# Kernel optimization log

Hardware: AMD Instinct MI355X
Metric: run time of the kernel (lower is better)

## Reference

```python
import jax, jax.numpy as jnp
import numpy as np

D_MODEL = 1024
N_HEAD = 16
D_K = 64
D_V = 64
LN_EPS = 1e-5


def setup_inputs() -> dict:
    key = jax.random.key(0)
    ks = jax.random.split(key, 12)
    B, S = 4, 2048
    s = 1.0 / np.sqrt(D_MODEL)
    inp = {
        "q": jax.random.normal(ks[0], (B, S, D_MODEL), jnp.float32),
        "k": jax.random.normal(ks[1], (B, S, D_MODEL), jnp.float32),
        "v": jax.random.normal(ks[2], (B, S, D_MODEL), jnp.float32),
        "mask": jnp.ones((B, S, S), jnp.int32),
        "w_q": jax.random.normal(ks[3], (D_MODEL, N_HEAD * D_K), jnp.float32) * s,
        "b_q": jnp.zeros((N_HEAD * D_K,), jnp.float32),
        "w_k": jax.random.normal(ks[4], (D_MODEL, N_HEAD * D_K), jnp.float32) * s,
        "b_k": jnp.zeros((N_HEAD * D_K,), jnp.float32),
        "w_v": jax.random.normal(ks[5], (D_MODEL, N_HEAD * D_V), jnp.float32) * s,
        "b_v": jnp.zeros((N_HEAD * D_V,), jnp.float32),
        "w_fc": jax.random.normal(ks[6], (N_HEAD * D_V, D_MODEL), jnp.float32) * s,
        "b_fc": jnp.zeros((D_MODEL,), jnp.float32),
        "ln_g": jnp.ones((D_MODEL,), jnp.float32),
        "ln_b": jnp.zeros((D_MODEL,), jnp.float32),
    }
    return inp


def reference(q, k, v, mask, w_q, b_q, w_k, b_k, w_v, b_v, w_fc, b_fc, ln_g, ln_b):
    B, Sq, _ = q.shape
    Sk = k.shape[1]
    residual = q
    # QKV projections -> [B, H, S, d]
    qh = (q @ w_q + b_q).reshape(B, Sq, N_HEAD, D_K).transpose(0, 2, 1, 3)
    kh = (k @ w_k + b_k).reshape(B, Sk, N_HEAD, D_K).transpose(0, 2, 1, 3)
    vh = (v @ w_v + b_v).reshape(B, Sk, N_HEAD, D_V).transpose(0, 2, 1, 3)
    temp = jnp.sqrt(jnp.asarray(D_K, qh.dtype))
    scores = jnp.einsum("bhqd,bhkd->bhqk", qh / temp, kh)
    scores = jnp.where(mask[:, None, :, :] == 0, jnp.asarray(-1e9, scores.dtype), scores)
    attn = jax.nn.softmax(scores, axis=-1)  # dropout is identity in eval
    out = jnp.einsum("bhqk,bhkd->bhqd", attn, vh)
    out = out.transpose(0, 2, 1, 3).reshape(B, Sq, N_HEAD * D_V)
    out = out @ w_fc + b_fc  # output proj (dropout identity)
    x = out + residual
    mu = jnp.mean(x, axis=-1, keepdims=True)
    var = jnp.mean(jnp.square(x - mu), axis=-1, keepdims=True)
    y = (x - mu) * jax.lax.rsqrt(var + LN_EPS) * ln_g + ln_b
    return (y, attn)
```

## Files before the change

kernel.cpp:

```cpp
#include <hip/hip_runtime.h>
#include <cstdint>
#include <cstddef>

#define DM 1024
#define HN 16
#define DH 64
#define BB 4
#define SS 2048
#define MM (BB * SS)

typedef __bf16 bf16;
typedef bf16 bf16x8 __attribute__((ext_vector_type(8)));
typedef bf16 bf16x4 __attribute__((ext_vector_type(4)));
typedef float f32x4 __attribute__((ext_vector_type(4)));

__device__ __forceinline__ f32x4 mfma16(bf16x8 a, bf16x8 b, f32x4 c) {
  return __builtin_amdgcn_mfma_f32_16x16x32_bf16(a, b, c, 0, 0, 0);
}

typedef __attribute__((address_space(3))) void lds_void_t;
typedef __attribute__((address_space(1))) void glob_void_t;

__device__ __forceinline__ void gload16(const void* g, void* l) {
  __builtin_amdgcn_global_load_lds((const glob_void_t*)g, (lds_void_t*)l, 16, 0, 0);
}

__global__ __launch_bounds__(256) void cvt_f2b(const float* __restrict__ in,
                                               bf16* __restrict__ out) {
  int i = (blockIdx.x * 256 + threadIdx.x) * 8;
  f32x4 a = *(const f32x4*)(in + i);
  f32x4 b = *(const f32x4*)(in + i + 4);
  bf16x8 o;
  o[0] = (bf16)a[0]; o[1] = (bf16)a[1]; o[2] = (bf16)a[2]; o[3] = (bf16)a[3];
  o[4] = (bf16)b[0]; o[5] = (bf16)b[1]; o[6] = (bf16)b[2]; o[7] = (bf16)b[3];
  *(bf16x8*)(out + i) = o;
}

__global__ __launch_bounds__(256) void wtrans(const float* __restrict__ W,
                                              bf16* __restrict__ WT) {
  __shared__ float t[32][33];
  int n0 = blockIdx.x * 32, k0 = blockIdx.y * 32;
  int tid = threadIdx.x;
  int r = tid >> 3, c = (tid & 7) * 4;
  f32x4 v = *(const f32x4*)&W[(size_t)(k0 + r) * DM + n0 + c];
  t[r][c] = v[0]; t[r][c + 1] = v[1]; t[r][c + 2] = v[2]; t[r][c + 3] = v[3];
  __syncthreads();
  bf16x4 o;
#pragma unroll
  for (int i = 0; i < 4; ++i) o[i] = (bf16)t[c + i][r];
  *(bf16x4*)&WT[(size_t)(n0 + r) * DM + k0 + c] = o;
}

__global__ __launch_bounds__(256) void vtrans(const bf16* __restrict__ vh,
                                              bf16* __restrict__ vhT) {
  __shared__ bf16 t[256][72];
  int bh = blockIdx.y, s0 = blockIdx.x * 256;
  const bf16* src = vh + (size_t)bh * SS * DH;
  bf16* dst = vhT + (size_t)bh * SS * DH;
  int tid = threadIdx.x;
#pragma unroll
  for (int j = 0; j < 8; ++j)
    *(bf16x8*)&t[tid][j * 8] = *(const bf16x8*)&src[(size_t)(s0 + tid) * DH + j * 8];
  __syncthreads();
  int d = tid >> 2, cc = (tid & 3) * 64;
#pragma unroll
  for (int j = 0; j < 8; ++j) {
    bf16x8 o;
#pragma unroll
    for (int i = 0; i < 8; ++i) o[i] = t[cc + j * 8 + i][d];
    *(bf16x8*)&dst[(size_t)d * SS + s0 + cc + j * 8] = o;
  }
}

template <int MODE>
__global__ __launch_bounds__(256) void gemm128(const bf16* __restrict__ A,
                                               const bf16* __restrict__ Bt,
                                               const float* __restrict__ bias,
                                               const float* __restrict__ resid,
                                               void* __restrict__ out) {
  constexpr int K = DM;
  __shared__ bf16 Ab[128 * 32];
  __shared__ bf16 Bb[128 * 32];
  int tid = threadIdx.x, wave = tid >> 6, lane = tid & 63;
  int bm = blockIdx.x * 128, bn = blockIdx.y * 128;
  int wr = (wave >> 1) * 64, wc = (wave & 1) * 64;
  int fr = lane & 15, kg8 = (lane >> 4) * 8;
  f32x4 acc[4][4] = {};
  int arow = tid >> 2, acol = (tid & 3) * 8;
  const bf16* Ag0 = A + (size_t)(bm + arow) * K + acol;
  const bf16* Ag1 = Ag0 + (size_t)64 * K;
  const bf16* Bg0 = Bt + (size_t)(bn + arow) * K + acol;
  const bf16* Bg1 = Bg0 + (size_t)64 * K;
  char* la = (char*)Ab + wave * 1024;
  char* lb = (char*)Bb + wave * 1024;
  for (int k0 = 0; k0 < K; k0 += 32) {
    __syncthreads();
    gload16(Ag0 + k0, la);
    gload16(Ag1 + k0, la + 4096);
    gload16(Bg0 + k0, lb);
    gload16(Bg1 + k0, lb + 4096);
    asm volatile("s_waitcnt vmcnt(0)" ::: "memory");
    __syncthreads();
    bf16x8 af[4], bfr[4];
#pragma unroll
    for (int m = 0; m < 4; ++m)
      af[m] = *(const bf16x8*)&Ab[(wr + m * 16 + fr) * 32 + kg8];
#pragma unroll
    for (int n = 0; n < 4; ++n)
      bfr[n] = *(const bf16x8*)&Bb[(wc + n * 16 + fr) * 32 + kg8];
#pragma unroll
    for (int m = 0; m < 4; ++m)
#pragma unroll
      for (int n = 0; n < 4; ++n) acc[m][n] = mfma16(af[m], bfr[n], acc[m][n]);
  }
#pragma unroll
  for (int m = 0; m < 4; ++m)
#pragma unroll
    for (int n = 0; n < 4; ++n) {
      int c = bn + wc + n * 16 + fr;
      float bv = bias[c];
#pragma unroll
      for (int j = 0; j < 4; ++j) {
        int r = bm + wr + m * 16 + (lane >> 4) * 4 + j;
        float v = acc[m][n][j] + bv;
        if (MODE == 0) {
          size_t idx = (size_t)((r >> 11) * HN + (c >> 6)) * (SS * DH) +
                       (size_t)(r & (SS - 1)) * DH + (c & (DH - 1));
          ((bf16*)out)[idx] = (bf16)v;
        } else {
          size_t idx = (size_t)r * DM + c;
          ((float*)out)[idx] = v + resid[idx];
        }
      }
    }
}

__global__ __launch_bounds__(512) void attn_kernel(const bf16* __restrict__ qh,
                                                   const bf16* __restrict__ kh,
                                                   const bf16* __restrict__ vhT,
                                                   const int* __restrict__ mask,
                                                   float* __restrict__ attn_out,
                                                   bf16* __restrict__ ctx) {
  extern __shared__ char smem[];
  float* pbuf = (float*)(smem + 16 * 4096);
  float* invp = (float*)(smem + 16 * 4096 + 4096);
  int tid = threadIdx.x, wave = tid >> 6, lane = tid & 63;
  int qt = blockIdx.x, bh = blockIdx.y;
  int b = bh >> 4, h = bh & 15;
  int q0 = qt * 16;
  const bf16* qbase = qh + ((size_t)bh * SS + q0) * DH;
  const bf16* kbase = kh + (size_t)bh * SS * DH;
  const bf16* vbase = vhT + (size_t)bh * SS * DH;
  int fr = lane & 15, kg = lane >> 4;

  bf16x8 qf0 = *(const bf16x8*)&qbase[(size_t)fr * DH + kg * 8];
  bf16x8 qf1 = *(const bf16x8*)&qbase[(size_t)fr * DH + 32 + kg * 8];

  int sw = wave * 256;
  const int* mrow = mask + ((size_t)b * SS + q0) * SS;
  for (int s0 = sw; s0 < sw + 256; s0 += 16) {
    f32x4 acc = {0.f, 0.f, 0.f, 0.f};
    bf16x8 kf0 = *(const bf16x8*)&kbase[(size_t)(s0 + fr) * DH + kg * 8];
    bf16x8 kf1 = *(const bf16x8*)&kbase[(size_t)(s0 + fr) * DH + 32 + kg * 8];
    acc = mfma16(qf0, kf0, acc);
    acc = mfma16(qf1, kf1, acc);
    int col = s0 + fr;
    int slot = col >> 3, within = col & 7;
#pragma unroll
    for (int j = 0; j < 4; ++j) {
      int row = kg * 4 + j;
      float v = acc[j] * 0.125f;
      if (mrow[(size_t)row * SS + col] == 0) v = -1e9f;
      *(bf16*)(smem + row * 4096 + ((slot ^ row) << 4) + within * 2) = (bf16)v;
    }
  }
  __syncthreads();

  {
    int row = wave * 2 + (lane >> 5);
    int la = lane & 31;
    char* rbase = smem + row * 4096;
    int rm = row;
    float mx = -1e30f;
#pragma unroll 2
    for (int it = 0; it < 8; ++it) {
      int slot = la + it * 32;
      bf16x8 e = *(const bf16x8*)(rbase + ((slot ^ rm) << 4));
#pragma unroll
      for (int i = 0; i < 8; ++i) mx = fmaxf(mx, (float)e[i]);
    }
#pragma unroll
    for (int off = 1; off < 32; off <<= 1) mx = fmaxf(mx, __shfl_xor(mx, off));
    float sum = 0.f;
#pragma unroll 2
    for (int it = 0; it < 8; ++it) {
      int slot = la + it * 32;
      char* p = rbase + ((slot ^ rm) << 4);
      bf16x8 e = *(const bf16x8*)p;
      bf16x8 w8;
#pragma unroll
      for (int i = 0; i < 8; ++i) {
        float f = __expf((float)e[i] - mx);
        sum += f;
        w8[i] = (bf16)f;
      }
      *(bf16x8*)p = w8;
    }
#pragma unroll
    for (int off = 1; off < 32; off <<= 1) sum += __shfl_xor(sum, off);
    float inv = 1.f / sum;
    if (la == 0) invp[row] = inv;
    float* arow_ = attn_out + ((size_t)bh * SS + q0 + row) * SS;
#pragma unroll 2
    for (int it = 0; it < 8; ++it) {
      int slot = la + it * 32;
      bf16x8 e = *(const bf16x8*)(rbase + ((slot ^ rm) << 4));
      f32x4 u0, u1;
#pragma unroll
      for (int i = 0; i < 4; ++i) {
        u0[i] = (float)e[i] * inv;
        u1[i] = (float)e[i + 4] * inv;
      }
      __builtin_nontemporal_store(u0, (f32x4*)&arow_[slot * 8]);
      __builtin_nontemporal_store(u1, (f32x4*)&arow_[slot * 8 + 4]);
    }
  }
  __syncthreads();

  {
    int dq = wave & 3, khalf = wave >> 2;
    f32x4 cacc = {0.f, 0.f, 0.f, 0.f};
    const bf16* vrow = vbase + (size_t)(dq * 16 + fr) * SS;
    char* prow = smem + fr * 4096;
    int prm = fr;
    for (int k0 = khalf * 1024; k0 < khalf * 1024 + 1024; k0 += 32) {
      int slotA = (k0 >> 3) + kg;
      bf16x8 pa = *(const bf16x8*)(prow + ((slotA ^ prm) << 4));
      bf16x8 vf = *(const bf16x8*)&vrow[k0 + kg * 8];
      cacc = mfma16(pa, vf, cacc);
    }
    if (khalf == 1) {
#pragma unroll
      for (int j = 0; j < 4; ++j)
        pbuf[dq * 256 + (kg * 4 + j) * 16 + fr] = cacc[j];
    }
    __syncthreads();
    if (khalf == 0) {
#pragma unroll
      for (int j = 0; j < 4; ++j) {
        int row = kg * 4 + j;
        float v = (cacc[j] + pbuf[dq * 256 + row * 16 + fr]) * invp[row];
        ctx[((size_t)b * SS + q0 + row) * DM + h * DH + dq * 16 + fr] = (bf16)v;
      }
    }
  }
}

__global__ __launch_bounds__(256) void ln_k(float* __restrict__ x,
                                            const float* __restrict__ g,
                                            const float* __restrict__ bln) {
  int r = blockIdx.x, tid = threadIdx.x;
  f32x4 v = *(const f32x4*)&x[(size_t)r * DM + tid * 4];
  float s = v[0] + v[1] + v[2] + v[3];
  float s2 = v[0] * v[0] + v[1] * v[1] + v[2] * v[2] + v[3] * v[3];
#pragma unroll
  for (int off = 32; off; off >>= 1) {
    s += __shfl_down(s, off);
    s2 += __shfl_down(s2, off);
  }
  __shared__ float rs_[4], rs2_[4];
  int wave = tid >> 6, lane = tid & 63;
  if (lane == 0) {
    rs_[wave] = s;
    rs2_[wave] = s2;
  }
  __syncthreads();
  s = rs_[0] + rs_[1] + rs_[2] + rs_[3];
  s2 = rs2_[0] + rs2_[1] + rs2_[2] + rs2_[3];
  float mu = s * (1.f / DM);
  float var = s2 * (1.f / DM) - mu * mu;
  float rstd = rsqrtf(var + 1e-5f);
  f32x4 gg = *(const f32x4*)&g[tid * 4];
  f32x4 bb = *(const f32x4*)&bln[tid * 4];
  f32x4 o;
#pragma unroll
  for (int i = 0; i < 4; ++i) o[i] = (v[i] - mu) * rstd * gg[i] + bb[i];
  *(f32x4*)&x[(size_t)r * DM + tid * 4] = o;
}

extern "C" void kernel_launch(void* const* d_in, const int* in_sizes, int n_in,
                              void* d_out, int out_size, void* d_ws,
                              size_t ws_size, hipStream_t stream) {
  const float* q = (const float*)d_in[0];
  const float* k = (const float*)d_in[1];
  const float* v = (const float*)d_in[2];
  const int* mask = (const int*)d_in[3];
  const float* w_q = (const float*)d_in[4];
  const float* b_q = (const float*)d_in[5];
  const float* w_k = (const float*)d_in[6];
  const float* b_k = (const float*)d_in[7];
  const float* w_v = (const float*)d_in[8];
  const float* b_v = (const float*)d_in[9];
  const float* w_fc = (const float*)d_in[10];
  const float* b_fc = (const float*)d_in[11];
  const float* ln_g = (const float*)d_in[12];
  const float* ln_b = (const float*)d_in[13];

  float* y = (float*)d_out;
  float* attn_out = (float*)d_out + (size_t)MM * DM;

  char* w = (char*)d_ws;
  const size_t actN = (size_t)MM * DM;
  bf16* q_bf = (bf16*)w;  w += actN * 2;
  bf16* k_bf = (bf16*)w;  w += actN * 2;
  bf16* v_bf = (bf16*)w;  w += actN * 2;
  bf16* wqT = (bf16*)w;   w += (size_t)DM * DM * 2;
  bf16* wkT = (bf16*)w;   w += (size_t)DM * DM * 2;
  bf16* wvT = (bf16*)w;   w += (size_t)DM * DM * 2;
  bf16* wfcT = (bf16*)w;  w += (size_t)DM * DM * 2;
  bf16* qhh = (bf16*)w;   w += actN * 2;
  bf16* khh = (bf16*)w;   w += actN * 2;
  bf16* vhh = (bf16*)w;   w += actN * 2;
  bf16* vhT = (bf16*)w;   w += actN * 2;
  bf16* ctx = (bf16*)w;   w += actN * 2;

  cvt_f2b<<<4096, 256, 0, stream>>>(q, q_bf);
  cvt_f2b<<<4096, 256, 0, stream>>>(k, k_bf);
  cvt_f2b<<<4096, 256, 0, stream>>>(v, v_bf);
  dim3 wg(DM / 32, DM / 32);
  wtrans<<<wg, 256, 0, stream>>>(w_q, wqT);
  wtrans<<<wg, 256, 0, stream>>>(w_k, wkT);
  wtrans<<<wg, 256, 0, stream>>>(w_v, wvT);
  wtrans<<<wg, 256, 0, stream>>>(w_fc, wfcT);
  dim3 gg(MM / 128, DM / 128);
  gemm128<0><<<gg, 256, 0, stream>>>(q_bf, wqT, b_q, nullptr, qhh);
  gemm128<0><<<gg, 256, 0, stream>>>(k_bf, wkT, b_k, nullptr, khh);
  gemm128<0><<<gg, 256, 0, stream>>>(v_bf, wvT, b_v, nullptr, vhh);
  vtrans<<<dim3(SS / 256, BB * HN), 256, 0, stream>>>(vhh, vhT);
  hipFuncSetAttribute((const void*)attn_kernel,
                      hipFuncAttributeMaxDynamicSharedMemorySize, 69696);
  attn_kernel<<<dim3(SS / 16, BB * HN), 512, 69696, stream>>>(
      qhh, khh, vhT, mask, attn_out, ctx);
  gemm128<1><<<gg, 256, 0, stream>>>(ctx, wfcT, b_fc, q, (void*)y);
  ln_k<<<MM, 256, 0, stream>>>(y, ln_g, ln_b);
}
```

Baseline: 805.2 us.

## Batch QKV projection, fuse V transpose, drop softmax max pass, prefetch attention loads

Merges the three input conversions, four weight transposes and three QKV GEMMs into single launches, with the GEMM picking its projection from the column block. The V projection epilogue writes the transposed layout directly, which removes the separate vtrans kernel, and the 1/8 scale is folded into Q. The softmax drops the max-subtraction pass and applies the mask as vectorized int loads in the exp pass. The QK and PV loops are software-pipelined with register prefetch, and the attention kernel gets an occupancy hint in its launch bounds. Skipping the max subtraction risks overflow for large scores, and a fully masked row would now divide by zero instead of giving a uniform distribution.

Result: faster. 759.0 us (-5.7%).

```diff
diff --git a/kernel.cpp b/kernel.cpp
--- a/kernel.cpp
+++ b/kernel.cpp
@@ -13,6 +13,7 @@
 typedef bf16 bf16x8 __attribute__((ext_vector_type(8)));
 typedef bf16 bf16x4 __attribute__((ext_vector_type(4)));
 typedef float f32x4 __attribute__((ext_vector_type(4)));
+typedef int i32x4 __attribute__((ext_vector_type(4)));
 
 __device__ __forceinline__ f32x4 mfma16(bf16x8 a, bf16x8 b, f32x4 c) {
   return __builtin_amdgcn_mfma_f32_16x16x32_bf16(a, b, c, 0, 0, 0);
@@ -25,8 +26,13 @@
   __builtin_amdgcn_global_load_lds((const glob_void_t*)g, (lds_void_t*)l, 16, 0, 0);
 }
 
-__global__ __launch_bounds__(256) void cvt_f2b(const float* __restrict__ in,
-                                               bf16* __restrict__ out) {
+__global__ __launch_bounds__(256) void cvt3(const float* __restrict__ q,
+                                            const float* __restrict__ k,
+                                            const float* __restrict__ v,
+                                            bf16* __restrict__ dst) {
+  int which = blockIdx.y;
+  const float* in = which == 0 ? q : which == 1 ? k : v;
+  bf16* out = dst + (size_t)which * MM * DM;
   int i = (blockIdx.x * 256 + threadIdx.x) * 8;
   f32x4 a = *(const f32x4*)(in + i);
   f32x4 b = *(const f32x4*)(in + i + 4);
@@ -36,8 +42,14 @@
   *(bf16x8*)(out + i) = o;
 }
 
-__global__ __launch_bounds__(256) void wtrans(const float* __restrict__ W,
-                                              bf16* __restrict__ WT) {
+__global__ __launch_bounds__(256) void wtrans4(const float* __restrict__ w_q,
+                                               const float* __restrict__ w_k,
+                                               const float* __restrict__ w_v,
+                                               const float* __restrict__ w_fc,
+                                               bf16* __restrict__ WT) {
+  int p = blockIdx.z;
+  const float* W = p == 0 ? w_q : p == 1 ? w_k : p == 2 ? w_v : w_fc;
+  bf16* out = WT + (size_t)p * DM * DM;
   __shared__ float t[32][33];
   int n0 = blockIdx.x * 32, k0 = blockIdx.y * 32;
   int tid = threadIdx.x;
@@ -48,36 +60,89 @@
   bf16x4 o;
 #pragma unroll
   for (int i = 0; i < 4; ++i) o[i] = (bf16)t[c + i][r];
-  *(bf16x4*)&WT[(size_t)(n0 + r) * DM + k0 + c] = o;
-}
-
-__global__ __launch_bounds__(256) void vtrans(const bf16* __restrict__ vh,
-                                              bf16* __restrict__ vhT) {
-  __shared__ bf16 t[256][72];
-  int bh = blockIdx.y, s0 = blockIdx.x * 256;
-  const bf16* src = vh + (size_t)bh * SS * DH;
-  bf16* dst = vhT + (size_t)bh * SS * DH;
-  int tid = threadIdx.x;
-#pragma unroll
-  for (int j = 0; j < 8; ++j)
-    *(bf16x8*)&t[tid][j * 8] = *(const bf16x8*)&src[(size_t)(s0 + tid) * DH + j * 8];
-  __syncthreads();
-  int d = tid >> 2, cc = (tid & 3) * 64;
-#pragma unroll
-  for (int j = 0; j < 8; ++j) {
-    bf16x8 o;
-#pragma unroll
-    for (int i = 0; i < 8; ++i) o[i] = t[cc + j * 8 + i][d];
-    *(bf16x8*)&dst[(size_t)d * SS + s0 + cc + j * 8] = o;
-  }
-}
-
-template <int MODE>
-__global__ __launch_bounds__(256) void gemm128(const bf16* __restrict__ A,
-                                               const bf16* __restrict__ Bt,
-                                               const float* __restrict__ bias,
-                                               const float* __restrict__ resid,
-                                               void* __restrict__ out) {
+  *(bf16x4*)&out[(size_t)(n0 + r) * DM + k0 + c] = o;
+}
+
+__global__ __launch_bounds__(256) void gemm_qkv(const bf16* __restrict__ Abase,
+                                                const bf16* __restrict__ Bt,
+                                                const float* __restrict__ b_q,
+                                                const float* __restrict__ b_k,
+                                                const float* __restrict__ b_v,
+                                                bf16* __restrict__ qhh,
+                                                bf16* __restrict__ khh,
+                                                bf16* __restrict__ vhT) {
+  constexpr int K = DM;
+  __shared__ bf16 Ab[128 * 32];
+  __shared__ bf16 Bb[128 * 32];
+  int tid = threadIdx.x, wave = tid >> 6, lane = tid & 63;
+  int bm = blockIdx.x * 128, bn = blockIdx.y * 128;
+  int proj = bn >> 10;
+  const bf16* A = Abase + (size_t)proj * MM * DM;
+  const float* bias = proj == 0 ? b_q : proj == 1 ? b_k : b_v;
+  int wr = (wave >> 1) * 64, wc = (wave & 1) * 64;
+  int fr = lane & 15, kg8 = (lane >> 4) * 8;
+  f32x4 acc[4][4] = {};
+  int arow = tid >> 2, acol = (tid & 3) * 8;
+  const bf16* Ag0 = A + (size_t)(bm + arow) * K + acol;
+  const bf16* Ag1 = Ag0 + (size_t)64 * K;
+  const bf16* Bg0 = Bt + (size_t)(bn + arow) * K + acol;
+  const bf16* Bg1 = Bg0 + (size_t)64 * K;
+  char* la = (char*)Ab + wave * 1024;
+  char* lb = (char*)Bb + wave * 1024;
+  for (int k0 = 0; k0 < K; k0 += 32) {
+    __syncthreads();
+    gload16(Ag0 + k0, la);
+    gload16(Ag1 + k0, la + 4096);
+    gload16(Bg0 + k0, lb);
+    gload16(Bg1 + k0, lb + 4096);
+    asm volatile("s_waitcnt vmcnt(0)" ::: "memory");
+    __syncthreads();
+    bf16x8 af[4], bfr[4];
+#pragma unroll
+    for (int m = 0; m < 4; ++m)
+      af[m] = *(const bf16x8*)&Ab[(wr + m * 16 + fr) * 32 + kg8];
+#pragma unroll
+    for (int n = 0; n < 4; ++n)
+      bfr[n] = *(const bf16x8*)&Bb[(wc + n * 16 + fr) * 32 + kg8];
+#pragma unroll
+    for (int m = 0; m < 4; ++m)
+#pragma unroll
+      for (int n = 0; n < 4; ++n) acc[m][n] = mfma16(af[m], bfr[n], acc[m][n]);
+  }
+  int b = bm >> 11;
+#pragma unroll
+  for (int m = 0; m < 4; ++m)
+#pragma unroll
+    for (int n = 0; n < 4; ++n) {
+      int c = bn + wc + n * 16 + fr;
+      int lc = c & 1023;
+      float bv = bias[lc];
+      int h = lc >> 6, d = lc & 63;
+      int r0 = bm + wr + m * 16 + (lane >> 4) * 4;
+      int s0 = r0 & (SS - 1);
+      if (proj == 2) {
+        bf16x4 o;
+#pragma unroll
+        for (int j = 0; j < 4; ++j) o[j] = (bf16)(acc[m][n][j] + bv);
+        *(bf16x4*)&vhT[((size_t)(b * HN + h) * DH + d) * SS + s0] = o;
+      } else {
+        bf16* dst = proj == 0 ? qhh : khh;
+        float sc = proj == 0 ? 0.125f : 1.f;
+#pragma unroll
+        for (int j = 0; j < 4; ++j) {
+          float v = (acc[m][n][j] + bv) * sc;
+          dst[(size_t)(b * HN + h) * (SS * DH) + (size_t)(s0 + j) * DH + d] =
+              (bf16)v;
+        }
+      }
+    }
+}
+
+__global__ __launch_bounds__(256) void gemm_out(const bf16* __restrict__ A,
+                                                const bf16* __restrict__ Bt,
+                                                const float* __restrict__ bias,
+                                                const float* __restrict__ resid,
+                                                float* __restrict__ out) {
   constexpr int K = DM;
   __shared__ bf16 Ab[128 * 32];
   __shared__ bf16 Bb[128 * 32];
@@ -122,25 +187,16 @@
 #pragma unroll
       for (int j = 0; j < 4; ++j) {
         int r = bm + wr + m * 16 + (lane >> 4) * 4 + j;
-        float v = acc[m][n][j] + bv;
-        if (MODE == 0) {
-          size_t idx = (size_t)((r >> 11) * HN + (c >> 6)) * (SS * DH) +
-                       (size_t)(r & (SS - 1)) * DH + (c & (DH - 1));
-          ((bf16*)out)[idx] = (bf16)v;
-        } else {
-          size_t idx = (size_t)r * DM + c;
-          ((float*)out)[idx] = v + resid[idx];
-        }
-      }
-    }
-}
-
-__global__ __launch_bounds__(512) void attn_kernel(const bf16* __restrict__ qh,
-                                                   const bf16* __restrict__ kh,
-                                                   const bf16* __restrict__ vhT,
-                                                   const int* __restrict__ mask,
-                                                   float* __restrict__ attn_out,
-                                                   bf16* __restrict__ ctx) {
+        size_t idx = (size_t)r * DM + c;
+        out[idx] = acc[m][n][j] + bv + resid[idx];
+      }
+    }
+}
+
+__global__ __launch_bounds__(512, 4) void attn_kernel(
+    const bf16* __restrict__ qh, const bf16* __restrict__ kh,
+    const bf16* __restrict__ vhT, const int* __restrict__ mask,
+    float* __restrict__ attn_out, bf16* __restrict__ ctx) {
   extern __shared__ char smem[];
   float* pbuf = (float*)(smem + 16 * 4096);
   float* invp = (float*)(smem + 16 * 4096 + 4096);
@@ -156,22 +212,31 @@
   bf16x8 qf0 = *(const bf16x8*)&qbase[(size_t)fr * DH + kg * 8];
   bf16x8 qf1 = *(const bf16x8*)&qbase[(size_t)fr * DH + 32 + kg * 8];
 
-  int sw = wave * 256;
-  const int* mrow = mask + ((size_t)b * SS + q0) * SS;
-  for (int s0 = sw; s0 < sw + 256; s0 += 16) {
-    f32x4 acc = {0.f, 0.f, 0.f, 0.f};
-    bf16x8 kf0 = *(const bf16x8*)&kbase[(size_t)(s0 + fr) * DH + kg * 8];
-    bf16x8 kf1 = *(const bf16x8*)&kbase[(size_t)(s0 + fr) * DH + 32 + kg * 8];
-    acc = mfma16(qf0, kf0, acc);
-    acc = mfma16(qf1, kf1, acc);
-    int col = s0 + fr;
-    int slot = col >> 3, within = col & 7;
-#pragma unroll
-    for (int j = 0; j < 4; ++j) {
-      int row = kg * 4 + j;
-      float v = acc[j] * 0.125f;
-      if (mrow[(size_t)row * SS + col] == 0) v = -1e9f;
-      *(bf16*)(smem + row * 4096 + ((slot ^ row) << 4) + within * 2) = (bf16)v;
+  {
+    int sw = wave * 256;
+    bf16x8 kb0[4], kb1[4];
+    auto kload = [&](int g) {
+      const bf16* kp = kbase + (size_t)(sw + g * 16 + fr) * DH + kg * 8;
+      kb0[g & 3] = *(const bf16x8*)kp;
+      kb1[g & 3] = *(const bf16x8*)(kp + 32);
+    };
+    kload(0);
+    kload(1);
+    kload(2);
+#pragma unroll
+    for (int g = 0; g < 16; ++g) {
+      if (g < 13) kload(g + 3);
+      f32x4 acc = {0.f, 0.f, 0.f, 0.f};
+      acc = mfma16(qf0, kb0[g & 3], acc);
+      acc = mfma16(qf1, kb1[g & 3], acc);
+      int col = sw + g * 16 + fr;
+      int slot = col >> 3, within = col & 7;
+#pragma unroll
+      for (int j = 0; j < 4; ++j) {
+        int row = kg * 4 + j;
+        *(bf16*)(smem + row * 4096 + ((slot ^ row) << 4) + within * 2) =
+            (bf16)acc[j];
+      }
     }
   }
   __syncthreads();
@@ -180,29 +245,29 @@
     int row = wave * 2 + (lane >> 5);
     int la = lane & 31;
     char* rbase = smem + row * 4096;
-    int rm = row;
-    float mx = -1e30f;
-#pragma unroll 2
+    const int* mrow = mask + ((size_t)b * SS + q0 + row) * SS;
+    float sum = 0.f;
+#pragma unroll
     for (int it = 0; it < 8; ++it) {
       int slot = la + it * 32;
-      bf16x8 e = *(const bf16x8*)(rbase + ((slot ^ rm) << 4));
-#pragma unroll
-      for (int i = 0; i < 8; ++i) mx = fmaxf(mx, (float)e[i]);
-    }
-#pragma unroll
-    for (int off = 1; off < 32; off <<= 1) mx = fmaxf(mx, __shfl_xor(mx, off));
-    float sum = 0.f;
-#pragma unroll 2
-    for (int it = 0; it < 8; ++it) {
-      int slot = la + it * 32;
-      char* p = rbase + ((slot ^ rm) << 4);
+      char* p = rbase + ((slot ^ row) << 4);
       bf16x8 e = *(const bf16x8*)p;
+      i32x4 ma = *(const i32x4*)&mrow[slot * 8];
+      i32x4 mb = *(const i32x4*)&mrow[slot * 8 + 4];
       bf16x8 w8;
 #pragma unroll
-      for (int i = 0; i < 8; ++i) {
-        float f = __expf((float)e[i] - mx);
+      for (int i = 0; i < 4; ++i) {
+        float f = __expf((float)e[i]);
+        f = (ma[i] == 0) ? 0.f : f;
         sum += f;
         w8[i] = (bf16)f;
+      }
+#pragma unroll
+      for (int i = 0; i < 4; ++i) {
+        float f = __expf((float)e[i + 4]);
+        f = (mb[i] == 0) ? 0.f : f;
+        sum += f;
+        w8[i + 4] = (bf16)f;
       }
       *(bf16x8*)p = w8;
     }
@@ -211,10 +276,10 @@
     float inv = 1.f / sum;
     if (la == 0) invp[row] = inv;
     float* arow_ = attn_out + ((size_t)bh * SS + q0 + row) * SS;
-#pragma unroll 2
+#pragma unroll
     for (int it = 0; it < 8; ++it) {
       int slot = la + it * 32;
-      bf16x8 e = *(const bf16x8*)(rbase + ((slot ^ rm) << 4));
+      bf16x8 e = *(const bf16x8*)(rbase + ((slot ^ row) << 4));
       f32x4 u0, u1;
 #pragma unroll
       for (int i = 0; i < 4; ++i) {
@@ -230,14 +295,21 @@
   {
     int dq = wave & 3, khalf = wave >> 2;
     f32x4 cacc = {0.f, 0.f, 0.f, 0.f};
-    const bf16* vrow = vbase + (size_t)(dq * 16 + fr) * SS;
+    const bf16* vrow = vbase + (size_t)(dq * 16 + fr) * SS + khalf * 1024;
     char* prow = smem + fr * 4096;
-    int prm = fr;
-    for (int k0 = khalf * 1024; k0 < khalf * 1024 + 1024; k0 += 32) {
-      int slotA = (k0 >> 3) + kg;
-      bf16x8 pa = *(const bf16x8*)(prow + ((slotA ^ prm) << 4));
-      bf16x8 vf = *(const bf16x8*)&vrow[k0 + kg * 8];
-      cacc = mfma16(pa, vf, cacc);
+    bf16x8 vb[4], pb[4];
+    auto pvload = [&](int kk) {
+      vb[kk & 3] = *(const bf16x8*)&vrow[kk * 32 + kg * 8];
+      int slotA = khalf * 128 + kk * 4 + kg;
+      pb[kk & 3] = *(const bf16x8*)(prow + ((slotA ^ fr) << 4));
+    };
+    pvload(0);
+    pvload(1);
+    pvload(2);
+#pragma unroll
+    for (int kk = 0; kk < 32; ++kk) {
+      if (kk < 29) pvload(kk + 3);
+      cacc = mfma16(pb[kk & 3], vb[kk & 3], cacc);
     }
     if (khalf == 1) {
 #pragma unroll
@@ -311,36 +383,22 @@
 
   char* w = (char*)d_ws;
   const size_t actN = (size_t)MM * DM;
-  bf16* q_bf = (bf16*)w;  w += actN * 2;
-  bf16* k_bf = (bf16*)w;  w += actN * 2;
-  bf16* v_bf = (bf16*)w;  w += actN * 2;
-  bf16* wqT = (bf16*)w;   w += (size_t)DM * DM * 2;
-  bf16* wkT = (bf16*)w;   w += (size_t)DM * DM * 2;
-  bf16* wvT = (bf16*)w;   w += (size_t)DM * DM * 2;
-  bf16* wfcT = (bf16*)w;  w += (size_t)DM * DM * 2;
-  bf16* qhh = (bf16*)w;   w += actN * 2;
-  bf16* khh = (bf16*)w;   w += actN * 2;
-  bf16* vhh = (bf16*)w;   w += actN * 2;
-  bf16* vhT = (bf16*)w;   w += actN * 2;
-  bf16* ctx = (bf16*)w;   w += actN * 2;
-
-  cvt_f2b<<<4096, 256, 0, stream>>>(q, q_bf);
-  cvt_f2b<<<4096, 256, 0, stream>>>(k, k_bf);
-  cvt_f2b<<<4096, 256, 0, stream>>>(v, v_bf);
-  dim3 wg(DM / 32, DM / 32);
-  wtrans<<<wg, 256, 0, stream>>>(w_q, wqT);
-  wtrans<<<wg, 256, 0, stream>>>(w_k, wkT);
-  wtrans<<<wg, 256, 0, stream>>>(w_v, wvT);
-  wtrans<<<wg, 256, 0, stream>>>(w_fc, wfcT);
-  dim3 gg(MM / 128, DM / 128);
-  gemm128<0><<<gg, 256, 0, stream>>>(q_bf, wqT, b_q, nullptr, qhh);
-  gemm128<0><<<gg, 256, 0, stream>>>(k_bf, wkT, b_k, nullptr, khh);
-  gemm128<0><<<gg, 256, 0, stream>>>(v_bf, wvT, b_v, nullptr, vhh);
-  vtrans<<<dim3(SS / 256, BB * HN), 256, 0, stream>>>(vhh, vhT);
+  bf16* qkv_bf = (bf16*)w;  w += 3 * actN * 2;
+  bf16* wT = (bf16*)w;      w += (size_t)4 * DM * DM * 2;
+  bf16* qhh = (bf16*)w;     w += actN * 2;
+  bf16* khh = (bf16*)w;     w += actN * 2;
+  bf16* vhT = (bf16*)w;     w += actN * 2;
+  bf16* ctx = (bf16*)w;     w += actN * 2;
+
+  cvt3<<<dim3(4096, 3), 256, 0, stream>>>(q, k, v, qkv_bf);
+  wtrans4<<<dim3(DM / 32, DM / 32, 4), 256, 0, stream>>>(w_q, w_k, w_v, w_fc, wT);
+  gemm_qkv<<<dim3(MM / 128, 3072 / 128), 256, 0, stream>>>(
+      qkv_bf, wT, b_q, b_k, b_v, qhh, khh, vhT);
   hipFuncSetAttribute((const void*)attn_kernel,
                       hipFuncAttributeMaxDynamicSharedMemorySize, 69696);
   attn_kernel<<<dim3(SS / 16, BB * HN), 512, 69696, stream>>>(
       qhh, khh, vhT, mask, attn_out, ctx);
-  gemm128<1><<<gg, 256, 0, stream>>>(ctx, wfcT, b_fc, q, (void*)y);
+  gemm_out<<<dim3(MM / 128, DM / 128), 256, 0, stream>>>(
+      ctx, wT + (size_t)3 * DM * DM, b_fc, q, y);
   ln_k<<<MM, 256, 0, stream>>>(y, ln_g, ln_b);
 }
```
